# Kernel optimization log

Measured on AMD Instinct MI355X. Metric: run time of the kernel, lower is better.

## Reference

```python
import jax, jax.numpy as jnp
import numpy as np

B, S, D, H = 16, 1024, 768, 12
HS = D // H  # head size = 64
NEG = -1000000.0  # module uses -1e6, not -inf


def setup_inputs() -> dict:
    key = jax.random.key(0)
    k1, k2, k3 = jax.random.split(key, 3)
    scale = 1.0 / np.sqrt(D)
    return {
        "x": jax.random.normal(k1, (B, S, D), dtype=jnp.float32),
        "W_qkv": jax.random.normal(k2, (D, 3 * D), dtype=jnp.float32) * scale,
        "b_qkv": jnp.zeros((3 * D,), dtype=jnp.float32),
        "W_o": jax.random.normal(k3, (D, D), dtype=jnp.float32) * scale,
        "b_o": jnp.zeros((D,), dtype=jnp.float32),
    }


def reference(x, W_qkv, b_qkv, W_o, b_o):
    qkv = x @ W_qkv + b_qkv                      # [B,S,3D]
    q, k, v = jnp.split(qkv, 3, axis=-1)         # each [B,S,D]
    q = q.reshape(B, S, H, HS)
    k = k.reshape(B, S, H, HS)
    v = v.reshape(B, S, H, HS)
    scores = jnp.einsum('bqhd,bkhd->bhqk', q, k) / np.sqrt(HS).astype(np.float32)
    causal = jnp.tril(jnp.ones((S, S), dtype=bool))
    scores = jnp.where(causal, scores, jnp.float32(NEG))
    probs = jax.nn.softmax(scores, axis=-1)      # dropout is eval-mode identity
    av = jnp.einsum('bhqk,bkhd->bqhd', probs, v).reshape(B, S, D)
    return av @ W_o + b_o
```

## Files before the change

### kernel.cpp

```cpp
#include <hip/hip_runtime.h>
#include <stdint.h>

typedef unsigned short u16;
typedef __attribute__((ext_vector_type(8))) short bf16x8;
typedef __attribute__((ext_vector_type(8))) u16 u16x8;
typedef __attribute__((ext_vector_type(4))) u16 u16x4;
typedef __attribute__((ext_vector_type(4))) float f32x4;
typedef __attribute__((ext_vector_type(16))) float f32x16;

#define B_ 16
#define S_ 1024
#define D_ 768
#define H_ 12

__device__ __forceinline__ float bf2f(u16 u) {
  unsigned int x = ((unsigned int)u) << 16;
  float f;
  __builtin_memcpy(&f, &x, 4);
  return f;
}
__device__ __forceinline__ u16 f2bf(float f) {
  unsigned int x;
  __builtin_memcpy(&x, &f, 4);
  x += 0x7fffu + ((x >> 16) & 1u);
  return (u16)(x >> 16);
}

#define MFMA16(a, b, c) __builtin_amdgcn_mfma_f32_16x16x32_bf16((a), (b), (c), 0, 0, 0)
#define MFMA32(a, b, c) __builtin_amdgcn_mfma_f32_32x32x16_bf16((a), (b), (c), 0, 0, 0)

#define GLD16(g, l)                                              \
  __builtin_amdgcn_global_load_lds(                              \
      (const __attribute__((address_space(1))) void*)(g),        \
      (__attribute__((address_space(3))) void*)(l), 16, 0, 0)

__global__ __launch_bounds__(256) void prep(const float* __restrict__ x,
                                            u16* __restrict__ xb,
                                            const float* __restrict__ Wqkv,
                                            u16* __restrict__ WqkvT,
                                            const float* __restrict__ Wo,
                                            u16* __restrict__ WoT) {
  __shared__ u16 tt[32][33];
  const int gx = blockIdx.x;
  const int tid = threadIdx.x;
  if (gx < 6144) {
    const int i = gx * 256 + tid;
    const float4 a = *(const float4*)(x + (size_t)i * 8);
    const float4 b = *(const float4*)(x + (size_t)i * 8 + 4);
    u16x8 o;
    o[0] = f2bf(a.x); o[1] = f2bf(a.y); o[2] = f2bf(a.z); o[3] = f2bf(a.w);
    o[4] = f2bf(b.x); o[5] = f2bf(b.y); o[6] = f2bf(b.z); o[7] = f2bf(b.w);
    *(u16x8*)(xb + (size_t)i * 8) = o;
  } else if (gx < 6144 + 1728) {
    const int t = gx - 6144;
    const int n0 = (t % 72) * 32, k0 = (t / 72) * 32;
    const int tx = tid & 31, ty = tid >> 5;
#pragma unroll
    for (int i = 0; i < 32; i += 8)
      tt[ty + i][tx] = f2bf(Wqkv[(size_t)(k0 + ty + i) * 2304 + n0 + tx]);
    __syncthreads();
#pragma unroll
    for (int i = 0; i < 32; i += 8)
      WqkvT[(size_t)(n0 + ty + i) * 768 + k0 + tx] = tt[tx][ty + i];
  } else {
    const int t = gx - 7872;
    const int n0 = (t % 24) * 32, k0 = (t / 24) * 32;
    const int tx = tid & 31, ty = tid >> 5;
#pragma unroll
    for (int i = 0; i < 32; i += 8)
      tt[ty + i][tx] = f2bf(Wo[(size_t)(k0 + ty + i) * 768 + n0 + tx]);
    __syncthreads();
#pragma unroll
    for (int i = 0; i < 32; i += 8)
      WoT[(size_t)(n0 + ty + i) * 768 + k0 + tx] = tt[tx][ty + i];
  }
}

template <int MODE>
__global__ __launch_bounds__(512, 4) void gemm_bt(const u16* __restrict__ A,
                                                  const u16* __restrict__ Bt,
                                                  const float* __restrict__ bias,
                                                  u16* __restrict__ O0, u16* __restrict__ O1,
                                                  u16* __restrict__ O2, float* __restrict__ Of,
                                                  int M, int N, int K) {
  __shared__ u16 Al[3 * 256 * 32];
  __shared__ u16 Bl[3 * 128 * 32];
  const int tid = threadIdx.x;
  const int wid = tid >> 6, lane = tid & 63;
  const int lo = lane & 15, hi = lane >> 4;
  const int wr = wid >> 1, wc = wid & 1;
  const int m0 = blockIdx.x * 256, n0 = blockIdx.y * 128;
  const int rA = lane >> 2;
  const int kc = (lane & 3) * 8;
  const int srow = wid * 16 + rA;
  f32x4 acc[4][4] = {};
  const int T = K >> 5;

  const u16* agp0 = A + (size_t)(m0 + srow) * K + kc;
  const u16* agp1 = A + (size_t)(m0 + srow + 128) * K + kc;
  const u16* bgp0 = Bt + (size_t)(n0 + srow) * K + kc;
  const int wb = wid * 1024;

#define STAGE(kt, buf)                                            \
  do {                                                            \
    const int _k0 = (kt) * 32;                                    \
    GLD16(agp0 + _k0, (char*)Al + (buf) * 16384 + wb);            \
    GLD16(agp1 + _k0, (char*)Al + (buf) * 16384 + 8192 + wb);     \
    GLD16(bgp0 + _k0, (char*)Bl + (buf) * 8192 + wb);             \
  } while (0)

  STAGE(0, 0);
  STAGE(1, 1);
  asm volatile("s_waitcnt vmcnt(3)" ::: "memory");
  __builtin_amdgcn_s_barrier();

  for (int t = 0; t < T; ++t) {
    if (t + 2 < T) STAGE(t + 2, (t + 2) % 3);
    const int ca = (t % 3) * 8192;
    const int cb = (t % 3) * 4096;
    bf16x8 af[4], bfr[4];
#pragma unroll
    for (int i = 0; i < 4; ++i)
      af[i] = *(const bf16x8*)&Al[ca + (wr * 64 + i * 16 + lo) * 32 + hi * 8];
#pragma unroll
    for (int j = 0; j < 4; ++j)
      bfr[j] = *(const bf16x8*)&Bl[cb + (wc * 64 + j * 16 + lo) * 32 + hi * 8];
    __builtin_amdgcn_s_setprio(1);
#pragma unroll
    for (int i = 0; i < 4; ++i)
#pragma unroll
      for (int j = 0; j < 4; ++j) acc[i][j] = MFMA16(af[i], bfr[j], acc[i][j]);
    __builtin_amdgcn_s_setprio(0);
    if (t + 2 < T) {
      asm volatile("s_waitcnt vmcnt(3)" ::: "memory");
    } else if (t + 1 < T) {
      asm volatile("s_waitcnt vmcnt(0)" ::: "memory");
    }
    __builtin_amdgcn_s_barrier();
  }
#undef STAGE
#pragma unroll
  for (int g = 0; g < 4; ++g) {
    const int n = n0 + wc * 64 + g * 16 + lo;
    const float bv = bias[n];
#pragma unroll
    for (int f = 0; f < 4; ++f) {
#pragma unroll
      for (int r = 0; r < 4; ++r) {
        const int m = m0 + wr * 64 + f * 16 + hi * 4 + r;
        const float fv = acc[f][g][r] + bv;
        if (MODE == 0) {
          const u16 o = f2bf(fv);
          if (n0 < D_) {
            O0[(size_t)m * D_ + n] = o;
          } else if (n0 < 2 * D_) {
            O1[(size_t)m * D_ + (n - D_)] = o;
          } else {
            const int np = n - 2 * D_;
            O2[(((size_t)(m >> 10) * H_ + (np >> 6)) * 64 + (np & 63)) * S_ + (m & 1023)] = o;
          }
        } else {
          Of[(size_t)m * N + n] = fv;
        }
      }
    }
  }
}

__global__ __launch_bounds__(256) void attn_fwd2(const u16* __restrict__ Qb,
                                                 const u16* __restrict__ Kb,
                                                 const u16* __restrict__ VTb,
                                                 u16* __restrict__ att) {
  __shared__ u16 Kl[2048];
  __shared__ u16 Vl[2048];
  const int tid = threadIdx.x;
  const int lane = tid & 63, wid = tid >> 6;
  const int l31 = lane & 31, hi1 = lane >> 5;
  const int L = blockIdx.x + 8 * (blockIdx.y + 12 * blockIdx.z);
  const int bx = (L >> 3) & 7;
  const int P = (L & 7) + 8 * (L >> 6);
  const int h = P % 12, b = P / 12;
  const int q0 = bx * 128;
  const int qw0 = q0 + wid * 32;
  const int qg = qw0 + l31;
  const size_t rowbase = (size_t)b * S_;

  bf16x8 qf[4];
  {
    const u16* qp = Qb + (rowbase + qg) * D_ + h * 64 + hi1 * 8;
#pragma unroll
    for (int c = 0; c < 4; ++c) {
      bf16x8 v = *(const bf16x8*)(qp + c * 16);
#pragma unroll
      for (int j = 0; j < 8; ++j) v[j] = (short)f2bf(bf2f((u16)v[j]) * 0.125f);
      qf[c] = v;
    }
  }
  float mrun = -3.0e38f, lrun = 0.0f;
  f32x16 o0 = {}, o1 = {};

  const u16* kgp =
      Kb + (rowbase + (tid & 31)) * D_ + h * 64 + (tid >> 6) * 16 + ((tid >> 5) & 1) * 8;
  const u16* vgp = VTb +
                   (((size_t)b * H_ + h) * 64 + ((tid >> 6) & 1) * 32 + (tid & 31)) * S_ +
                   (tid >> 7) * 16 + ((tid >> 5) & 1) * 8;
  char* kdst = (char*)Kl + wid * 1024;
  char* vdst = (char*)Vl + wid * 1024;
  const char* kbase = (const char*)Kl + lane * 16;
  const char* vbase = (const char*)Vl + lane * 16;

  const int kvend = q0 + 128;
  for (int kv0 = 0; kv0 < kvend; kv0 += 32) {
    __syncthreads();
    GLD16(kgp + (size_t)kv0 * D_, kdst);
    GLD16(vgp + kv0, vdst);
    __syncthreads();
    if (kv0 > qw0 + 31) continue;

    f32x16 s = {};
#pragma unroll
    for (int c = 0; c < 4; ++c) s = MFMA32(*(const bf16x8*)(kbase + c * 1024), qf[c], s);

    if (kv0 + 31 > qw0) {
#pragma unroll
      for (int r = 0; r < 16; ++r) {
        const int kvg = kv0 + (r & 3) + 8 * (r >> 2) + 4 * hi1;
        if (kvg > qg) s[r] = -1.0e30f;
      }
    }
    float rm = s[0];
#pragma unroll
    for (int r = 1; r < 16; ++r) rm = fmaxf(rm, s[r]);
    rm = fmaxf(rm, __shfl_xor(rm, 32));
    const float mn = fmaxf(mrun, rm);
    const float fr = __expf(mrun - mn);
    mrun = mn;
    float p[16];
    float rs = 0.0f;
#pragma unroll
    for (int r = 0; r < 16; ++r) {
      p[r] = __expf(s[r] - mn);
      rs += p[r];
    }
    rs += __shfl_xor(rs, 32);
    lrun = lrun * fr + rs;
#pragma unroll
    for (int r = 0; r < 16; ++r) {
      o0[r] *= fr;
      o1[r] *= fr;
    }
    unsigned int pa[4], pb[4];
#pragma unroll
    for (int g = 0; g < 4; ++g) {
      pa[g] = (unsigned)f2bf(p[4 * g]) | ((unsigned)f2bf(p[4 * g + 1]) << 16);
      pb[g] = (unsigned)f2bf(p[4 * g + 2]) | ((unsigned)f2bf(p[4 * g + 3]) << 16);
    }
    const unsigned sa = __shfl_xor(hi1 ? pa[0] : pa[1], 32);
    const unsigned sb = __shfl_xor(hi1 ? pb[0] : pb[1], 32);
    const unsigned sc = __shfl_xor(hi1 ? pa[2] : pa[3], 32);
    const unsigned sd = __shfl_xor(hi1 ? pb[2] : pb[3], 32);
    const uint4 w0 = hi1 ? make_uint4(sa, sb, pa[1], pb[1]) : make_uint4(pa[0], pb[0], sa, sb);
    const uint4 w1 = hi1 ? make_uint4(sc, sd, pa[3], pb[3]) : make_uint4(pa[2], pb[2], sc, sd);
    bf16x8 pf0, pf1;
    __builtin_memcpy(&pf0, &w0, 16);
    __builtin_memcpy(&pf1, &w1, 16);
    o0 = MFMA32(*(const bf16x8*)(vbase + 0 * 1024), pf0, o0);
    o1 = MFMA32(*(const bf16x8*)(vbase + 1 * 1024), pf0, o1);
    o0 = MFMA32(*(const bf16x8*)(vbase + 2 * 1024), pf1, o0);
    o1 = MFMA32(*(const bf16x8*)(vbase + 3 * 1024), pf1, o1);
  }
  const float inv = 1.0f / lrun;
  u16* op = att + (rowbase + qg) * D_ + h * 64;
#pragma unroll
  for (int g = 0; g < 4; ++g) {
    u16x4 v0, v1;
#pragma unroll
    for (int j = 0; j < 4; ++j) {
      v0[j] = f2bf(o0[4 * g + j] * inv);
      v1[j] = f2bf(o1[4 * g + j] * inv);
    }
    *(u16x4*)(op + 8 * g + 4 * hi1) = v0;
    *(u16x4*)(op + 32 + 8 * g + 4 * hi1) = v1;
  }
}

extern "C" void kernel_launch(void* const* d_in, const int* in_sizes, int n_in, void* d_out,
                              int out_size, void* d_ws, size_t ws_size, hipStream_t stream) {
  const float *x = nullptr, *Wqkv = nullptr, *bqkv = nullptr, *Wo = nullptr, *bo = nullptr;
  for (int i = 0; i < n_in; ++i) {
    switch (in_sizes[i]) {
      case 16384 * 768:  x = (const float*)d_in[i]; break;
      case 768 * 2304:   Wqkv = (const float*)d_in[i]; break;
      case 2304:         bqkv = (const float*)d_in[i]; break;
      case 768 * 768:    Wo = (const float*)d_in[i]; break;
      case 768:          bo = (const float*)d_in[i]; break;
    }
  }
  float* out = (float*)d_out;

  char* ws = (char*)d_ws;
  u16* WqkvT = (u16*)(ws);
  u16* WoT = (u16*)(ws + 3538944);
  u16* Qb = (u16*)(ws + 4718592);
  u16* Kb = (u16*)(ws + 29884416);
  u16* VT = (u16*)(ws + 55050240);
  u16* xb = (u16*)d_out;
  u16* att = Qb;

  prep<<<8448, 256, 0, stream>>>(x, xb, Wqkv, WqkvT, Wo, WoT);
  gemm_bt<0><<<dim3(64, 18), 512, 0, stream>>>(xb, WqkvT, bqkv, Qb, Kb, VT, nullptr,
                                               16384, 2304, 768);
  attn_fwd2<<<dim3(8, H_, B_), 256, 0, stream>>>(Qb, Kb, VT, att);
  gemm_bt<1><<<dim3(64, 6), 512, 0, stream>>>(att, WoT, bo, nullptr, nullptr, nullptr, out,
                                              16384, 768, 768);
}
```

Measured before the change: 261.3 us.

## Fuse x-to-bf16 conversion into QKV GEMM with row-stationary LDS tiles

Drops the separate fp32-to-bf16 pass over x and converts x on the fly inside the QKV projection kernel. Both GEMMs are rewritten so each 256-thread block holds a 32-row strip of A (all 768 K) in LDS while each wave streams its share of the transposed weights straight from global memory into registers. This removes one full read and write of the activation tensor but gives up LDS reuse of the weight tiles. It also launches only 512 blocks with small 32-row tiles, so weights are re-read per block and MFMA utilisation may fall.

Measured after the change: 611.5 us. 2.34x slower.

```diff
diff --git a/kernel.cpp b/kernel.cpp
--- a/kernel.cpp
+++ b/kernel.cpp
@@ -34,27 +34,16 @@
       (const __attribute__((address_space(1))) void*)(g),        \
       (__attribute__((address_space(3))) void*)(l), 16, 0, 0)
 
-__global__ __launch_bounds__(256) void prep(const float* __restrict__ x,
-                                            u16* __restrict__ xb,
-                                            const float* __restrict__ Wqkv,
+__global__ __launch_bounds__(256) void prep(const float* __restrict__ Wqkv,
                                             u16* __restrict__ WqkvT,
                                             const float* __restrict__ Wo,
                                             u16* __restrict__ WoT) {
   __shared__ u16 tt[32][33];
   const int gx = blockIdx.x;
   const int tid = threadIdx.x;
-  if (gx < 6144) {
-    const int i = gx * 256 + tid;
-    const float4 a = *(const float4*)(x + (size_t)i * 8);
-    const float4 b = *(const float4*)(x + (size_t)i * 8 + 4);
-    u16x8 o;
-    o[0] = f2bf(a.x); o[1] = f2bf(a.y); o[2] = f2bf(a.z); o[3] = f2bf(a.w);
-    o[4] = f2bf(b.x); o[5] = f2bf(b.y); o[6] = f2bf(b.z); o[7] = f2bf(b.w);
-    *(u16x8*)(xb + (size_t)i * 8) = o;
-  } else if (gx < 6144 + 1728) {
-    const int t = gx - 6144;
-    const int n0 = (t % 72) * 32, k0 = (t / 72) * 32;
-    const int tx = tid & 31, ty = tid >> 5;
+  const int tx = tid & 31, ty = tid >> 5;
+  if (gx < 1728) {
+    const int n0 = (gx % 72) * 32, k0 = (gx / 72) * 32;
 #pragma unroll
     for (int i = 0; i < 32; i += 8)
       tt[ty + i][tx] = f2bf(Wqkv[(size_t)(k0 + ty + i) * 2304 + n0 + tx]);
@@ -63,9 +52,8 @@
     for (int i = 0; i < 32; i += 8)
       WqkvT[(size_t)(n0 + ty + i) * 768 + k0 + tx] = tt[tx][ty + i];
   } else {
-    const int t = gx - 7872;
+    const int t = gx - 1728;
     const int n0 = (t % 24) * 32, k0 = (t / 24) * 32;
-    const int tx = tid & 31, ty = tid >> 5;
 #pragma unroll
     for (int i = 0; i < 32; i += 8)
       tt[ty + i][tx] = f2bf(Wo[(size_t)(k0 + ty + i) * 768 + n0 + tx]);
@@ -77,90 +65,92 @@
 }
 
 template <int MODE>
-__global__ __launch_bounds__(512, 4) void gemm_bt(const u16* __restrict__ A,
-                                                  const u16* __restrict__ Bt,
-                                                  const float* __restrict__ bias,
-                                                  u16* __restrict__ O0, u16* __restrict__ O1,
-                                                  u16* __restrict__ O2, float* __restrict__ Of,
-                                                  int M, int N, int K) {
-  __shared__ u16 Al[3 * 256 * 32];
-  __shared__ u16 Bl[3 * 128 * 32];
+__global__ __launch_bounds__(256, 3) void gemmAS(const float* __restrict__ xf,
+                                                 const u16* __restrict__ Ab,
+                                                 const u16* __restrict__ Wt,
+                                                 const float* __restrict__ bias,
+                                                 u16* __restrict__ O0, u16* __restrict__ O1,
+                                                 u16* __restrict__ O2,
+                                                 float* __restrict__ Of) {
+  constexpr int NTOT = (MODE == 0) ? 2304 : 768;
+  constexpr int NW = NTOT / 4;
+  constexpr int NCH = NW / 64;
+  __shared__ u16 X[48 * 64 * 8];
   const int tid = threadIdx.x;
   const int wid = tid >> 6, lane = tid & 63;
   const int lo = lane & 15, hi = lane >> 4;
-  const int wr = wid >> 1, wc = wid & 1;
-  const int m0 = blockIdx.x * 256, n0 = blockIdx.y * 128;
-  const int rA = lane >> 2;
-  const int kc = (lane & 3) * 8;
-  const int srow = wid * 16 + rA;
-  f32x4 acc[4][4] = {};
-  const int T = K >> 5;
-
-  const u16* agp0 = A + (size_t)(m0 + srow) * K + kc;
-  const u16* agp1 = A + (size_t)(m0 + srow + 128) * K + kc;
-  const u16* bgp0 = Bt + (size_t)(n0 + srow) * K + kc;
-  const int wb = wid * 1024;
-
-#define STAGE(kt, buf)                                            \
-  do {                                                            \
-    const int _k0 = (kt) * 32;                                    \
-    GLD16(agp0 + _k0, (char*)Al + (buf) * 16384 + wb);            \
-    GLD16(agp1 + _k0, (char*)Al + (buf) * 16384 + 8192 + wb);     \
-    GLD16(bgp0 + _k0, (char*)Bl + (buf) * 8192 + wb);             \
-  } while (0)
-
-  STAGE(0, 0);
-  STAGE(1, 1);
-  asm volatile("s_waitcnt vmcnt(3)" ::: "memory");
-  __builtin_amdgcn_s_barrier();
-
-  for (int t = 0; t < T; ++t) {
-    if (t + 2 < T) STAGE(t + 2, (t + 2) % 3);
-    const int ca = (t % 3) * 8192;
-    const int cb = (t % 3) * 4096;
-    bf16x8 af[4], bfr[4];
-#pragma unroll
-    for (int i = 0; i < 4; ++i)
-      af[i] = *(const bf16x8*)&Al[ca + (wr * 64 + i * 16 + lo) * 32 + hi * 8];
-#pragma unroll
-    for (int j = 0; j < 4; ++j)
-      bfr[j] = *(const bf16x8*)&Bl[cb + (wc * 64 + j * 16 + lo) * 32 + hi * 8];
-    __builtin_amdgcn_s_setprio(1);
-#pragma unroll
-    for (int i = 0; i < 4; ++i)
-#pragma unroll
-      for (int j = 0; j < 4; ++j) acc[i][j] = MFMA16(af[i], bfr[j], acc[i][j]);
-    __builtin_amdgcn_s_setprio(0);
-    if (t + 2 < T) {
-      asm volatile("s_waitcnt vmcnt(3)" ::: "memory");
-    } else if (t + 1 < T) {
-      asm volatile("s_waitcnt vmcnt(0)" ::: "memory");
-    }
-    __builtin_amdgcn_s_barrier();
-  }
-#undef STAGE
-#pragma unroll
-  for (int g = 0; g < 4; ++g) {
-    const int n = n0 + wc * 64 + g * 16 + lo;
-    const float bv = bias[n];
-#pragma unroll
-    for (int f = 0; f < 4; ++f) {
-#pragma unroll
-      for (int r = 0; r < 4; ++r) {
-        const int m = m0 + wr * 64 + f * 16 + hi * 4 + r;
-        const float fv = acc[f][g][r] + bv;
-        if (MODE == 0) {
-          const u16 o = f2bf(fv);
-          if (n0 < D_) {
-            O0[(size_t)m * D_ + n] = o;
-          } else if (n0 < 2 * D_) {
-            O1[(size_t)m * D_ + (n - D_)] = o;
+  const int m0 = blockIdx.x * 32;
+
+#pragma unroll
+  for (int s = 0; s < 12; ++s) {
+    const int id = s * 256 + tid;
+    const int c = id >> 6, l = id & 63;
+    const int row = (c & 1) * 16 + (l & 15);
+    const int k0 = (c >> 1) * 32 + (l >> 4) * 8;
+    u16x8 v;
+    if (MODE == 0) {
+      const float4 a = *(const float4*)(xf + (size_t)(m0 + row) * 768 + k0);
+      const float4 b = *(const float4*)(xf + (size_t)(m0 + row) * 768 + k0 + 4);
+      v[0] = f2bf(a.x); v[1] = f2bf(a.y); v[2] = f2bf(a.z); v[3] = f2bf(a.w);
+      v[4] = f2bf(b.x); v[5] = f2bf(b.y); v[6] = f2bf(b.z); v[7] = f2bf(b.w);
+    } else {
+      v = *(const u16x8*)(Ab + (size_t)(m0 + row) * 768 + k0);
+    }
+    *(u16x8*)&X[id * 8] = v;
+  }
+  __syncthreads();
+
+  for (int ch = 0; ch < NCH; ++ch) {
+    const int n0 = wid * NW + ch * 64;
+    const u16* wp = Wt + (size_t)(n0 + lo) * 768 + hi * 8;
+    f32x4 acc[2][4] = {};
+    bf16x8 ca0 = *(const bf16x8*)&X[(0 * 64 + lane) * 8];
+    bf16x8 ca1 = *(const bf16x8*)&X[(1 * 64 + lane) * 8];
+    bf16x8 cb[4];
+#pragma unroll
+    for (int g = 0; g < 4; ++g) cb[g] = *(const bf16x8*)(wp + (size_t)g * 16 * 768);
+    for (int k = 0; k < 24; ++k) {
+      bf16x8 na0, na1, nb[4];
+      if (k + 1 < 24) {
+        na0 = *(const bf16x8*)&X[(((k + 1) * 2 + 0) * 64 + lane) * 8];
+        na1 = *(const bf16x8*)&X[(((k + 1) * 2 + 1) * 64 + lane) * 8];
+#pragma unroll
+        for (int g = 0; g < 4; ++g)
+          nb[g] = *(const bf16x8*)(wp + (size_t)g * 16 * 768 + (k + 1) * 32);
+      }
+#pragma unroll
+      for (int g = 0; g < 4; ++g) {
+        acc[0][g] = MFMA16(ca0, cb[g], acc[0][g]);
+        acc[1][g] = MFMA16(ca1, cb[g], acc[1][g]);
+      }
+      ca0 = na0;
+      ca1 = na1;
+#pragma unroll
+      for (int g = 0; g < 4; ++g) cb[g] = nb[g];
+    }
+#pragma unroll
+    for (int g = 0; g < 4; ++g) {
+      const int n = n0 + g * 16 + lo;
+      const float bv = bias[n];
+#pragma unroll
+      for (int f = 0; f < 2; ++f) {
+#pragma unroll
+        for (int r = 0; r < 4; ++r) {
+          const int m = m0 + f * 16 + hi * 4 + r;
+          const float fv = acc[f][g][r] + bv;
+          if (MODE == 0) {
+            const u16 o = f2bf(fv);
+            if (n < D_) {
+              O0[(size_t)m * D_ + n] = o;
+            } else if (n < 2 * D_) {
+              O1[(size_t)m * D_ + (n - D_)] = o;
+            } else {
+              const int np = n - 2 * D_;
+              O2[(((size_t)(m >> 10) * H_ + (np >> 6)) * 64 + (np & 63)) * S_ + (m & 1023)] = o;
+            }
           } else {
-            const int np = n - 2 * D_;
-            O2[(((size_t)(m >> 10) * H_ + (np >> 6)) * 64 + (np & 63)) * S_ + (m & 1023)] = o;
+            Of[(size_t)m * D_ + n] = fv;
           }
-        } else {
-          Of[(size_t)m * N + n] = fv;
         }
       }
     }
@@ -304,13 +294,10 @@
   u16* Qb = (u16*)(ws + 4718592);
   u16* Kb = (u16*)(ws + 29884416);
   u16* VT = (u16*)(ws + 55050240);
-  u16* xb = (u16*)d_out;
   u16* att = Qb;
 
-  prep<<<8448, 256, 0, stream>>>(x, xb, Wqkv, WqkvT, Wo, WoT);
-  gemm_bt<0><<<dim3(64, 18), 512, 0, stream>>>(xb, WqkvT, bqkv, Qb, Kb, VT, nullptr,
-                                               16384, 2304, 768);
+  prep<<<2304, 256, 0, stream>>>(Wqkv, WqkvT, Wo, WoT);
+  gemmAS<0><<<512, 256, 0, stream>>>(x, nullptr, WqkvT, bqkv, Qb, Kb, VT, nullptr);
   attn_fwd2<<<dim3(8, H_, B_), 256, 0, stream>>>(Qb, Kb, VT, att);
-  gemm_bt<1><<<dim3(64, 6), 512, 0, stream>>>(att, WoT, bo, nullptr, nullptr, nullptr, out,
-                                              16384, 768, 768);
-}
+  gemmAS<1><<<512, 256, 0, stream>>>(nullptr, att, WoT, bo, nullptr, nullptr, nullptr, out);
+}
```

## Restructure GEMM to 128x128 tiles, BK=64, double buffering and XOR-swizzled LDS

Applied to the files above, without the earlier changes.

Changes the bf16 GEMM from a 256x128 tile with 512 threads, a K-step of 32 and triple buffering to a 128x128 tile with 256 threads, a K-step of 64 and double buffering. LDS rows are XOR-swizzled so that 16-byte fragment reads avoid bank conflicts. Each wave now issues twice as many MFMAs per barrier, which is meant to cut barrier and LDS overhead. In exchange the grid doubles, A/B reuse per tile drops, and with only two buffers each iteration waits with vmcnt(0), so prefetch overlap is shallower.

Measured after the change: 260.1 us. About the same (-0.5%).

```diff
diff --git a/kernel.cpp b/kernel.cpp
--- a/kernel.cpp
+++ b/kernel.cpp
@@ -77,65 +77,72 @@
 }
 
 template <int MODE>
-__global__ __launch_bounds__(512, 4) void gemm_bt(const u16* __restrict__ A,
+__global__ __launch_bounds__(256, 2) void gemm_bt(const u16* __restrict__ A,
                                                   const u16* __restrict__ Bt,
                                                   const float* __restrict__ bias,
                                                   u16* __restrict__ O0, u16* __restrict__ O1,
                                                   u16* __restrict__ O2, float* __restrict__ Of,
                                                   int M, int N, int K) {
-  __shared__ u16 Al[3 * 256 * 32];
-  __shared__ u16 Bl[3 * 128 * 32];
+  __shared__ u16 Al[2 * 128 * 64];
+  __shared__ u16 Bl[2 * 128 * 64];
   const int tid = threadIdx.x;
   const int wid = tid >> 6, lane = tid & 63;
   const int lo = lane & 15, hi = lane >> 4;
   const int wr = wid >> 1, wc = wid & 1;
-  const int m0 = blockIdx.x * 256, n0 = blockIdx.y * 128;
-  const int rA = lane >> 2;
-  const int kc = (lane & 3) * 8;
-  const int srow = wid * 16 + rA;
+  const int m0 = blockIdx.x * 128, n0 = blockIdx.y * 128;
+  const int T = K >> 6;
+
+  const int sr = lane >> 3;
+  const int kk = ((lane & 7) ^ sr) * 8;
+  const u16* const asrc = A + (size_t)(m0 + wid * 8 + sr) * K + kk;
+  const u16* const bsrc = Bt + (size_t)(n0 + wid * 8 + sr) * K + kk;
+
+#define STAGE(kt, buf)                                                          \
+  do {                                                                          \
+    const size_t _k = (size_t)(kt) * 64;                                        \
+    GLD16(asrc + _k, (char*)Al + (buf) * 16384 + (wid) * 1024);                 \
+    GLD16(asrc + (size_t)32 * K + _k, (char*)Al + (buf) * 16384 + (wid + 4) * 1024);  \
+    GLD16(asrc + (size_t)64 * K + _k, (char*)Al + (buf) * 16384 + (wid + 8) * 1024);  \
+    GLD16(asrc + (size_t)96 * K + _k, (char*)Al + (buf) * 16384 + (wid + 12) * 1024); \
+    GLD16(bsrc + _k, (char*)Bl + (buf) * 16384 + (wid) * 1024);                 \
+    GLD16(bsrc + (size_t)32 * K + _k, (char*)Bl + (buf) * 16384 + (wid + 4) * 1024);  \
+    GLD16(bsrc + (size_t)64 * K + _k, (char*)Bl + (buf) * 16384 + (wid + 8) * 1024);  \
+    GLD16(bsrc + (size_t)96 * K + _k, (char*)Bl + (buf) * 16384 + (wid + 12) * 1024); \
+  } while (0)
+
   f32x4 acc[4][4] = {};
-  const int T = K >> 5;
-
-  const u16* agp0 = A + (size_t)(m0 + srow) * K + kc;
-  const u16* agp1 = A + (size_t)(m0 + srow + 128) * K + kc;
-  const u16* bgp0 = Bt + (size_t)(n0 + srow) * K + kc;
-  const int wb = wid * 1024;
-
-#define STAGE(kt, buf)                                            \
-  do {                                                            \
-    const int _k0 = (kt) * 32;                                    \
-    GLD16(agp0 + _k0, (char*)Al + (buf) * 16384 + wb);            \
-    GLD16(agp1 + _k0, (char*)Al + (buf) * 16384 + 8192 + wb);     \
-    GLD16(bgp0 + _k0, (char*)Bl + (buf) * 8192 + wb);             \
-  } while (0)
 
   STAGE(0, 0);
-  STAGE(1, 1);
-  asm volatile("s_waitcnt vmcnt(3)" ::: "memory");
+  asm volatile("s_waitcnt vmcnt(0)" ::: "memory");
   __builtin_amdgcn_s_barrier();
 
   for (int t = 0; t < T; ++t) {
-    if (t + 2 < T) STAGE(t + 2, (t + 2) % 3);
-    const int ca = (t % 3) * 8192;
-    const int cb = (t % 3) * 4096;
-    bf16x8 af[4], bfr[4];
+    if (t + 1 < T) STAGE(t + 1, (t + 1) & 1);
+    const int cb = (t & 1) * 16384;
+    const int swz = (lo & 7) << 4;
+    bf16x8 af[4][2], bfv[4][2];
 #pragma unroll
     for (int i = 0; i < 4; ++i)
-      af[i] = *(const bf16x8*)&Al[ca + (wr * 64 + i * 16 + lo) * 32 + hi * 8];
+#pragma unroll
+      for (int s = 0; s < 2; ++s)
+        af[i][s] = *(const bf16x8*)((const char*)Al + cb + (wr * 64 + i * 16 + lo) * 128 +
+                                    ((s * 64 + hi * 16) ^ swz));
 #pragma unroll
     for (int j = 0; j < 4; ++j)
-      bfr[j] = *(const bf16x8*)&Bl[cb + (wc * 64 + j * 16 + lo) * 32 + hi * 8];
+#pragma unroll
+      for (int s = 0; s < 2; ++s)
+        bfv[j][s] = *(const bf16x8*)((const char*)Bl + cb + (wc * 64 + j * 16 + lo) * 128 +
+                                     ((s * 64 + hi * 16) ^ swz));
     __builtin_amdgcn_s_setprio(1);
 #pragma unroll
     for (int i = 0; i < 4; ++i)
 #pragma unroll
-      for (int j = 0; j < 4; ++j) acc[i][j] = MFMA16(af[i], bfr[j], acc[i][j]);
+      for (int j = 0; j < 4; ++j) {
+        acc[i][j] = MFMA16(af[i][0], bfv[j][0], acc[i][j]);
+        acc[i][j] = MFMA16(af[i][1], bfv[j][1], acc[i][j]);
+      }
     __builtin_amdgcn_s_setprio(0);
-    if (t + 2 < T) {
-      asm volatile("s_waitcnt vmcnt(3)" ::: "memory");
-    } else if (t + 1 < T) {
-      asm volatile("s_waitcnt vmcnt(0)" ::: "memory");
-    }
+    if (t + 1 < T) asm volatile("s_waitcnt vmcnt(0)" ::: "memory");
     __builtin_amdgcn_s_barrier();
   }
 #undef STAGE
@@ -308,9 +315,9 @@
   u16* att = Qb;
 
   prep<<<8448, 256, 0, stream>>>(x, xb, Wqkv, WqkvT, Wo, WoT);
-  gemm_bt<0><<<dim3(64, 18), 512, 0, stream>>>(xb, WqkvT, bqkv, Qb, Kb, VT, nullptr,
-                                               16384, 2304, 768);
+  gemm_bt<0><<<dim3(128, 18), 256, 0, stream>>>(xb, WqkvT, bqkv, Qb, Kb, VT, nullptr,
+                                                16384, 2304, 768);
   attn_fwd2<<<dim3(8, H_, B_), 256, 0, stream>>>(Qb, Kb, VT, att);
-  gemm_bt<1><<<dim3(64, 6), 512, 0, stream>>>(att, WoT, bo, nullptr, nullptr, nullptr, out,
-                                              16384, 768, 768);
-}
+  gemm_bt<1><<<dim3(128, 6), 256, 0, stream>>>(att, WoT, bo, nullptr, nullptr, nullptr, out,
+                                               16384, 768, 768);
+}
```
